# Kernel tuning notes

Measured on AMD Instinct MI355X. Metric: run time of the kernel, lower is better.

The kernel has to match this reference:

```python
import jax, jax.numpy as jnp
import numpy as np

# (dy, dx) offsets corresponding to the single -1 entries of kernels 1..8
# delta1 rows: (0,0),(0,1),(0,2),(1,2); delta2 = spatial flip: (2,2),(2,1),(2,0),(1,0)
OFFSETS = [(-1, -1), (-1, 0), (-1, 1), (0, 1), (1, 1), (1, 0), (1, -1), (0, -1)]
NUM_LAYER = 9
EPS = 1e-12


def _shift(x, dy, dx):
    # zero-padded shift: out[y, x] = in[y + dy, x + dx]; dilation = shifts[0] = 1
    b, c, h, w = x.shape
    p = jnp.pad(x, ((0, 0), (0, 0), (1, 1), (1, 1)))
    return jax.lax.dynamic_slice(p, (0, 0, 1 + dy, 1 + dx), (b, c, h, w))


def _l2norm(v, axis):
    # matches torch.nn.functional.normalize: v / max(||v||, eps)
    n = jnp.sqrt(jnp.sum(v * v, axis=axis, keepdims=True))
    return v / jnp.maximum(n, EPS)


def setup_inputs() -> dict:
    key = jax.random.key(0)
    k1, k2, k3, k4 = jax.random.split(key, 4)
    B, C, H, W = 4, 256, 96, 96
    cen = jax.random.normal(k1, (B, C, H, W), dtype=jnp.float32)
    scale = 1.0 / np.sqrt(C)
    # grouped 1x1 convs (groups=9): per-group (C x C) weight matrices
    W1 = jax.random.normal(k2, (NUM_LAYER, C, C), dtype=jnp.float32) * scale
    W2 = jax.random.normal(k3, (C, C), dtype=jnp.float32) * scale
    W3 = jax.random.normal(k4, (NUM_LAYER, C, C), dtype=jnp.float32) * scale
    return {"cen": cen, "W1": W1, "W2": W2, "W3": W3}


def reference(cen, W1, W2, W3):
    b, c, h, w = cen.shape
    # Extract_layer: 8 fixed depthwise 3x3 convs (each = negated shift) + identity
    surrounds = jnp.stack(
        [-_shift(cen, dy, dx) for dy, dx in OFFSETS] + [cen], axis=1
    )  # (b, 9, c, h, w)
    # Analyze_layer: grouped 1x1 convs = per-group matmuls
    out1 = jnp.einsum("gij,bgjhw->bgihw", W1, surrounds)
    out2 = jnp.einsum("ij,bjhw->bihw", W2, cen)[:, None]  # (b, 1, c, h, w)
    out3 = jnp.einsum("gij,bgjhw->bgihw", W3, surrounds)
    out1 = _l2norm(out1, axis=2)
    out2 = _l2norm(out2, axis=2)
    out3 = _l2norm(out3, axis=2)
    # softmax over a size-1 axis (dim=2 after mean+keepdim) -> identically 1.0
    att = jax.nn.softmax(
        jnp.mean(out1 * out2, axis=2, keepdims=True), axis=2
    )  # (b, 9, 1, h, w)
    out = jnp.sum(att * out3, axis=1)  # (b, c, h, w)
    return out + cen
```

## Files before the change

### kernel.cpp

```cpp
#include <hip/hip_runtime.h>
#include <stdint.h>

#define BB 4
#define CC 256
#define HH 96
#define WW 96
#define HP 98
#define CP 264
#define XT 32
#define YT 2
#define XE 34

typedef __bf16 bf16x8 __attribute__((ext_vector_type(8)));
typedef float f32x4 __attribute__((ext_vector_type(4)));
typedef float f32x16 __attribute__((ext_vector_type(16)));

__device__ __forceinline__ uint16_t f2bf(float f) {
    uint32_t u = __float_as_uint(f);
    u += 0x7FFFu + ((u >> 16) & 1u);
    return (uint16_t)(u >> 16);
}

__global__ void transpose_cen(const float* __restrict__ cen, uint16_t* __restrict__ cenT) {
    const int y = blockIdx.x, b = blockIdx.y, ch = blockIdx.z, tid = threadIdx.x;
    __shared__ uint16_t ldsX[128 * 100];

    #pragma unroll
    for (int i = 0; i < 12; ++i) {
        int f = i * 256 + tid;
        int c = f / 24, xq = f % 24;
        float4 v = *(const float4*)(cen + ((((size_t)b * CC + ch * 128 + c) * HH + y) * WW + xq * 4));
        uint2 pk;
        pk.x = (uint32_t)f2bf(v.x) | ((uint32_t)f2bf(v.y) << 16);
        pk.y = (uint32_t)f2bf(v.z) | ((uint32_t)f2bf(v.w) << 16);
        *(uint2*)(&ldsX[c * 100 + xq * 4]) = pk;
    }
    __syncthreads();
    #pragma unroll
    for (int i = 0; i < 6; ++i) {
        int t = i * 256 + tid;
        int x = t % 96, cq = t / 96;
        uint32_t w0, w1, w2, w3;
        w0 = (uint32_t)ldsX[(cq * 8 + 0) * 100 + x] | ((uint32_t)ldsX[(cq * 8 + 1) * 100 + x] << 16);
        w1 = (uint32_t)ldsX[(cq * 8 + 2) * 100 + x] | ((uint32_t)ldsX[(cq * 8 + 3) * 100 + x] << 16);
        w2 = (uint32_t)ldsX[(cq * 8 + 4) * 100 + x] | ((uint32_t)ldsX[(cq * 8 + 5) * 100 + x] << 16);
        w3 = (uint32_t)ldsX[(cq * 8 + 6) * 100 + x] | ((uint32_t)ldsX[(cq * 8 + 7) * 100 + x] << 16);
        size_t o = (((size_t)b * HP + (y + 1)) * HP + (x + 1)) * CP + ch * 128 + cq * 8;
        *(uint4*)(cenT + o) = make_uint4(w0, w1, w2, w3);
    }
}

__global__ void cvt_w3(const float* __restrict__ W3, uint16_t* __restrict__ W3bf) {
    int e = (blockIdx.x * 256 + threadIdx.x) * 4;
    int g = e >> 16, n = (e >> 8) & 255, k = e & 255;
    float4 v = *(const float4*)(W3 + e);
    uint2 pk;
    pk.x = (uint32_t)f2bf(v.x) | ((uint32_t)f2bf(v.y) << 16);
    pk.y = (uint32_t)f2bf(v.z) | ((uint32_t)f2bf(v.w) << 16);
    size_t o = (size_t)(((g * 8 + (n >> 5)) * 16 + (k >> 4)) * 512)
             + (n & 31) * 16 + ((k >> 3) & 1) * 8 + (k & 7);
    *(uint2*)(W3bf + o) = pk;
}

__global__ __launch_bounds__(256, 3)
void ecm_main(const float* __restrict__ cen, const uint16_t* __restrict__ cenT,
              const uint16_t* __restrict__ W3bf, float* __restrict__ out) {
    const int tid = threadIdx.x;
    const int wv = tid >> 6, lane = tid & 63, col = lane & 31, kh = lane >> 5;
    const int x0 = blockIdx.x * XT, y0 = blockIdx.y * YT, b = blockIdx.z;

    __shared__ __align__(16) uint16_t ldsA[YT * XE * CP];
    __shared__ __align__(16) float ldsP[2][64][4];

    const int dgOrd[9] = {0, 1, 2, 7, 8, 3, 6, 5, 4};

    const uint16_t* wbA = W3bf + (size_t)(2 * wv) * (16 * 512) + col * 16 + kh * 8;
    f32x16 finA0 = {}, finA1 = {}, finB0 = {}, finB1 = {};

    #pragma unroll 1
    for (int idx = 0; idx < 9; ++idx) {
        const int g = dgOrd[idx], dg = idx / 3, dx = idx % 3 - 1;

        if (idx % 3 == 0) {
            for (int r = 0; r < YT; ++r) {
                const uint4* gs = (const uint4*)(cenT + (((size_t)b * HP + (y0 + dg + r)) * HP + x0) * CP);
                uint4* ls = (uint4*)(ldsA + r * XE * CP);
                for (int c = tid; c < XE * CP / 8; c += 256) ls[c] = gs[c];
            }
            __syncthreads();
        }

        const uint16_t* wgA = wbA + (size_t)g * 65536;
        const uint16_t* wgB = wgA + 16 * 512;
        const int a0 = (col + dx + 1) * CP + kh * 8;
        const int a1 = a0 + XE * CP;

        f32x16 aA0 = {}, aA1 = {}, aB0 = {}, aB1 = {};
        bf16x8 wfA = *(const bf16x8*)(wgA);
        bf16x8 wfB = *(const bf16x8*)(wgB);
        bf16x8 b0 = *(const bf16x8*)(ldsA + a0);
        bf16x8 b1 = *(const bf16x8*)(ldsA + a1);
        #pragma unroll
        for (int ks = 0; ks < 15; ++ks) {
            bf16x8 wnA = *(const bf16x8*)(wgA + (ks + 1) * 512);
            bf16x8 wnB = *(const bf16x8*)(wgB + (ks + 1) * 512);
            bf16x8 bn0 = *(const bf16x8*)(ldsA + a0 + (ks + 1) * 16);
            bf16x8 bn1 = *(const bf16x8*)(ldsA + a1 + (ks + 1) * 16);
            aA0 = __builtin_amdgcn_mfma_f32_32x32x16_bf16(wfA, b0, aA0, 0, 0, 0);
            aB0 = __builtin_amdgcn_mfma_f32_32x32x16_bf16(wfB, b0, aB0, 0, 0, 0);
            aA1 = __builtin_amdgcn_mfma_f32_32x32x16_bf16(wfA, b1, aA1, 0, 0, 0);
            aB1 = __builtin_amdgcn_mfma_f32_32x32x16_bf16(wfB, b1, aB1, 0, 0, 0);
            wfA = wnA; wfB = wnB; b0 = bn0; b1 = bn1;
        }
        aA0 = __builtin_amdgcn_mfma_f32_32x32x16_bf16(wfA, b0, aA0, 0, 0, 0);
        aB0 = __builtin_amdgcn_mfma_f32_32x32x16_bf16(wfB, b0, aB0, 0, 0, 0);
        aA1 = __builtin_amdgcn_mfma_f32_32x32x16_bf16(wfA, b1, aA1, 0, 0, 0);
        aB1 = __builtin_amdgcn_mfma_f32_32x32x16_bf16(wfB, b1, aB1, 0, 0, 0);

        float s0 = 0.f, s1 = 0.f;
        #pragma unroll
        for (int r = 0; r < 16; ++r) {
            s0 += aA0[r] * aA0[r] + aB0[r] * aB0[r];
            s1 += aA1[r] * aA1[r] + aB1[r] * aB1[r];
        }
        s0 += __shfl_xor(s0, 32, 64);
        s1 += __shfl_xor(s1, 32, 64);
        if (kh == 0) { ldsP[idx & 1][col][wv] = s0; ldsP[idx & 1][32 + col][wv] = s1; }
        __syncthreads();

        f32x4 pa = *(const f32x4*)&ldsP[idx & 1][col][0];
        f32x4 qa = *(const f32x4*)&ldsP[idx & 1][32 + col][0];
        float n0 = pa[0] + pa[1] + pa[2] + pa[3];
        float n1 = qa[0] + qa[1] + qa[2] + qa[3];
        const float sgn = (g == 8) ? 1.f : -1.f;
        float sc0 = sgn / fmaxf(sqrtf(n0), 1e-12f);
        float sc1 = sgn / fmaxf(sqrtf(n1), 1e-12f);
        #pragma unroll
        for (int r = 0; r < 16; ++r) {
            finA0[r] += aA0[r] * sc0; finB0[r] += aB0[r] * sc0;
            finA1[r] += aA1[r] * sc1; finB1[r] += aB1[r] * sc1;
        }
    }

    #pragma unroll
    for (int r = 0; r < 16; ++r) {
        int chA = wv * 64 + (r & 3) + 8 * (r >> 2) + 4 * kh;
        size_t oA0 = (((size_t)b * CC + chA) * HH + y0) * WW + (x0 + col);
        size_t oA1 = oA0 + WW;
        out[oA0] = finA0[r] + cen[oA0];
        out[oA1] = finA1[r] + cen[oA1];
        size_t oB0 = oA0 + (size_t)32 * HH * WW;
        size_t oB1 = oB0 + WW;
        out[oB0] = finB0[r] + cen[oB0];
        out[oB1] = finB1[r] + cen[oB1];
    }
}

extern "C" void kernel_launch(void* const* d_in, const int* in_sizes, int n_in,
                              void* d_out, int out_size, void* d_ws, size_t ws_size,
                              hipStream_t stream) {
    const float* cen = (const float*)d_in[0];
    const float* W3 = (const float*)d_in[3];
    float* out = (float*)d_out;

    uint16_t* cenT = (uint16_t*)d_ws;
    const size_t cenT_elems = (size_t)BB * HP * HP * CP;
    uint16_t* W3bf = cenT + cenT_elems;

    hipMemsetAsync(d_ws, 0, cenT_elems * sizeof(uint16_t), stream);
    transpose_cen<<<dim3(HH, BB, 2), 256, 0, stream>>>(cen, cenT);
    cvt_w3<<<576, 256, 0, stream>>>(W3, W3bf);
    ecm_main<<<dim3(3, 48, 4), 256, 0, stream>>>(cen, cenT, W3bf, out);
}
```

Before: 171.9 us.

## Zero only halo of padded buffer and deepen MFMA operand prefetch

The full-buffer hipMemsetAsync over the padded bf16 activation workspace is replaced by a small kernel that zeroes only the one-pixel border. Every interior pixel is overwritten by the transpose kernel anyway, so this removes a large redundant write. The main GEMM loop now prefetches weight fragments four k-steps ahead and LDS activation fragments two steps ahead, to better hide global and LDS latency behind the MFMAs. The launch-bounds minimum is lowered from 3 to 2 blocks per CU, which allows more registers but may reduce occupancy.

```diff
diff --git a/kernel.cpp b/kernel.cpp
--- a/kernel.cpp
+++ b/kernel.cpp
@@ -19,6 +19,20 @@
     uint32_t u = __float_as_uint(f);
     u += 0x7FFFu + ((u >> 16) & 1u);
     return (uint16_t)(u >> 16);
+}
+
+__global__ void zero_halo(uint16_t* __restrict__ cenT) {
+    int idx = blockIdx.x * 256 + threadIdx.x;
+    if (idx >= 1552 * 33) return;
+    int p = idx / 33, q = idx - p * 33;
+    int b = p / 388, s = p - b * 388;
+    int y, x;
+    if (s < 98)      { y = 0;       x = s; }
+    else if (s < 196){ y = 97;      x = s - 98; }
+    else if (s < 292){ x = 0;       y = s - 196 + 1; }
+    else             { x = 97;      y = s - 292 + 1; }
+    size_t o = (((size_t)b * HP + y) * HP + x) * CP + q * 8;
+    *(uint4*)(cenT + o) = make_uint4(0u, 0u, 0u, 0u);
 }
 
 __global__ void transpose_cen(const float* __restrict__ cen, uint16_t* __restrict__ cenT) {
@@ -62,7 +76,7 @@
     *(uint2*)(W3bf + o) = pk;
 }
 
-__global__ __launch_bounds__(256, 3)
+__global__ __launch_bounds__(256, 2)
 void ecm_main(const float* __restrict__ cen, const uint16_t* __restrict__ cenT,
               const uint16_t* __restrict__ W3bf, float* __restrict__ out) {
     const int tid = threadIdx.x;
@@ -96,26 +110,36 @@
         const int a1 = a0 + XE * CP;
 
         f32x16 aA0 = {}, aA1 = {}, aB0 = {}, aB1 = {};
-        bf16x8 wfA = *(const bf16x8*)(wgA);
-        bf16x8 wfB = *(const bf16x8*)(wgB);
-        bf16x8 b0 = *(const bf16x8*)(ldsA + a0);
-        bf16x8 b1 = *(const bf16x8*)(ldsA + a1);
+
+        bf16x8 A0[4], A1[4], Bq0[2], Bq1[2];
         #pragma unroll
-        for (int ks = 0; ks < 15; ++ks) {
-            bf16x8 wnA = *(const bf16x8*)(wgA + (ks + 1) * 512);
-            bf16x8 wnB = *(const bf16x8*)(wgB + (ks + 1) * 512);
-            bf16x8 bn0 = *(const bf16x8*)(ldsA + a0 + (ks + 1) * 16);
-            bf16x8 bn1 = *(const bf16x8*)(ldsA + a1 + (ks + 1) * 16);
-            aA0 = __builtin_amdgcn_mfma_f32_32x32x16_bf16(wfA, b0, aA0, 0, 0, 0);
-            aB0 = __builtin_amdgcn_mfma_f32_32x32x16_bf16(wfB, b0, aB0, 0, 0, 0);
-            aA1 = __builtin_amdgcn_mfma_f32_32x32x16_bf16(wfA, b1, aA1, 0, 0, 0);
-            aB1 = __builtin_amdgcn_mfma_f32_32x32x16_bf16(wfB, b1, aB1, 0, 0, 0);
-            wfA = wnA; wfB = wnB; b0 = bn0; b1 = bn1;
+        for (int i = 0; i < 4; ++i) {
+            A0[i] = *(const bf16x8*)(wgA + i * 512);
+            A1[i] = *(const bf16x8*)(wgB + i * 512);
         }
-        aA0 = __builtin_amdgcn_mfma_f32_32x32x16_bf16(wfA, b0, aA0, 0, 0, 0);
-        aB0 = __builtin_amdgcn_mfma_f32_32x32x16_bf16(wfB, b0, aB0, 0, 0, 0);
-        aA1 = __builtin_amdgcn_mfma_f32_32x32x16_bf16(wfA, b1, aA1, 0, 0, 0);
-        aB1 = __builtin_amdgcn_mfma_f32_32x32x16_bf16(wfB, b1, aB1, 0, 0, 0);
+        #pragma unroll
+        for (int i = 0; i < 2; ++i) {
+            Bq0[i] = *(const bf16x8*)(ldsA + a0 + i * 16);
+            Bq1[i] = *(const bf16x8*)(ldsA + a1 + i * 16);
+        }
+
+        #pragma unroll
+        for (int ks = 0; ks < 16; ++ks) {
+            bf16x8 wa = A0[ks & 3], wb = A1[ks & 3];
+            bf16x8 v0 = Bq0[ks & 1], v1 = Bq1[ks & 1];
+            if (ks + 4 < 16) {
+                A0[ks & 3] = *(const bf16x8*)(wgA + (ks + 4) * 512);
+                A1[ks & 3] = *(const bf16x8*)(wgB + (ks + 4) * 512);
+            }
+            if (ks + 2 < 16) {
+                Bq0[ks & 1] = *(const bf16x8*)(ldsA + a0 + (ks + 2) * 16);
+                Bq1[ks & 1] = *(const bf16x8*)(ldsA + a1 + (ks + 2) * 16);
+            }
+            aA0 = __builtin_amdgcn_mfma_f32_32x32x16_bf16(wa, v0, aA0, 0, 0, 0);
+            aB0 = __builtin_amdgcn_mfma_f32_32x32x16_bf16(wb, v0, aB0, 0, 0, 0);
+            aA1 = __builtin_amdgcn_mfma_f32_32x32x16_bf16(wa, v1, aA1, 0, 0, 0);
+            aB1 = __builtin_amdgcn_mfma_f32_32x32x16_bf16(wb, v1, aB1, 0, 0, 0);
+        }
 
         float s0 = 0.f, s1 = 0.f;
         #pragma unroll
@@ -167,7 +191,7 @@
     const size_t cenT_elems = (size_t)BB * HP * HP * CP;
     uint16_t* W3bf = cenT + cenT_elems;
 
-    hipMemsetAsync(d_ws, 0, cenT_elems * sizeof(uint16_t), stream);
+    zero_halo<<<201, 256, 0, stream>>>(cenT);
     transpose_cen<<<dim3(HH, BB, 2), 256, 0, stream>>>(cen, cenT);
     cvt_w3<<<576, 256, 0, stream>>>(W3, W3bf);
     ecm_main<<<dim3(3, 48, 4), 256, 0, stream>>>(cen, cenT, W3bf, out);
```

Measured after the change: 195.1 us. 1.13x slower.
